# Kernel tuning notes

Measured on AMD Instinct MI355X. Metric: run time of the kernel, lower is better.

The kernel has to match this reference:

```python
import jax, jax.numpy as jnp
import numpy as np

N_NODES = 100000

def gcn_conv(x, edge_index, W, b, n_nodes):
    # GCNConv: out = D^{-1/2} (A + I) D^{-1/2} X W + b  (self-loops added)
    src, dst = edge_index[0], edge_index[1]
    loops = jnp.arange(n_nodes, dtype=edge_index.dtype)
    src = jnp.concatenate([src, loops])
    dst = jnp.concatenate([dst, loops])
    deg = jax.ops.segment_sum(jnp.ones_like(dst, dtype=x.dtype), dst, num_segments=n_nodes)
    dinv = jnp.where(deg > 0, jax.lax.rsqrt(deg), 0.0)
    norm = dinv[src] * dinv[dst]  # [E+N]
    h = x @ W  # transform first (small d), then gather/scatter
    msgs = h[src] * norm[:, None]
    out = jax.ops.segment_sum(msgs, dst, num_segments=n_nodes)
    return out + b


def setup_inputs() -> dict:
    key = jax.random.key(0)
    k1, k2, k3, k4, k5, k6 = jax.random.split(key, 6)
    x = jax.random.normal(k1, (N_NODES, 3), dtype=jnp.float32)
    edge_index = jax.random.randint(k2, (2, 2400000), 0, N_NODES, dtype=jnp.int64)
    # Glorot-style init for GCNConv linear weights; zero bias matches PyG default
    W1 = jax.random.normal(k3, (3, 16), dtype=jnp.float32) * (1.0 / np.sqrt(3))
    b1 = jnp.zeros((16,), dtype=jnp.float32)
    W2 = jax.random.normal(k4, (16, 32), dtype=jnp.float32) * (1.0 / np.sqrt(16))
    b2 = jnp.zeros((32,), dtype=jnp.float32)
    return {"x": x, "edge_index": edge_index, "W1": W1, "b1": b1, "W2": W2, "b2": b2}


def reference(x, edge_index, W1, b1, W2, b2):
    n = x.shape[0]
    h = gcn_conv(x, edge_index, W1, b1, n)
    h = jax.nn.relu(h)
    h = gcn_conv(h, edge_index, W2, b2, n)
    # batch is all zeros in the original forward -> single-graph mean pool
    return jnp.mean(h, axis=0, keepdims=True)  # [1, 32]
```

## Files before the change

### kernel.cpp

```cpp
#include <hip/hip_runtime.h>

typedef unsigned int uint;
typedef unsigned long long ull;


#define MAXB  256
#define CAP   16384u
#define BINB  512
#define CHUNK 4096
#define SPL   8
#define PADN  131072
#define AFS   2048.0f
#define AFB   16384
#define AFM   0x1FFFFFu

__device__ __forceinline__ uint slice_lo(uint c, uint s) {
    return (s == 0u) ? 0u : ((c * s / SPL) & ~7u);
}
__device__ __forceinline__ uint slice_hi(uint c, uint s) {
    return (s == SPL - 1u) ? c : ((c * (s + 1u) / SPL) & ~7u);
}

__global__ void __launch_bounds__(BINB)
bin_kernel(const int* __restrict__ key, const int* __restrict__ other,
           uint* __restrict__ cursor, uint* __restrict__ buf, int E) {
    __shared__ uint cnt[MAXB], scanb[MAXB], baseb[MAXB];
    __shared__ uint stage[CHUNK];
    const int tid = threadIdx.x;
    const int e0 = blockIdx.x * CHUNK;
    const int nE = min(CHUNK, E - e0);
    const int my0 = tid * 8;
    const int myc = max(0, min(8, nE - my0));
    if (tid < MAXB) cnt[tid] = 0u;

    uint k8[8], o8[8], r8[8];
    if (myc == 8) {
        int4 ka = ((const int4*)(key + e0))[tid * 2];
        int4 kb = ((const int4*)(key + e0))[tid * 2 + 1];
        int4 oa = ((const int4*)(other + e0))[tid * 2];
        int4 ob = ((const int4*)(other + e0))[tid * 2 + 1];
        k8[0] = ka.x; k8[1] = ka.y; k8[2] = ka.z; k8[3] = ka.w;
        k8[4] = kb.x; k8[5] = kb.y; k8[6] = kb.z; k8[7] = kb.w;
        o8[0] = oa.x; o8[1] = oa.y; o8[2] = oa.z; o8[3] = oa.w;
        o8[4] = ob.x; o8[5] = ob.y; o8[6] = ob.z; o8[7] = ob.w;
    } else {
        for (int r = 0; r < myc; ++r) {
            k8[r] = (uint)key[e0 + my0 + r];
            o8[r] = (uint)other[e0 + my0 + r];
        }
    }
    __syncthreads();
    for (int r = 0; r < myc; ++r) r8[r] = atomicAdd(&cnt[k8[r] >> 9], 1u);
    __syncthreads();
    if (tid < MAXB) scanb[tid] = cnt[tid];
    __syncthreads();
    for (int d = 1; d < MAXB; d <<= 1) {
        uint t = (tid < MAXB && tid >= d) ? scanb[tid - d] : 0u;
        __syncthreads();
        if (tid < MAXB) scanb[tid] += t;
        __syncthreads();
    }
    if (tid < MAXB) baseb[tid] = (uint)tid * CAP + (cnt[tid] ? atomicAdd(&cursor[tid * 16], cnt[tid]) : 0u);
    __syncthreads();
    for (int r = 0; r < myc; ++r) {
        uint b = k8[r] >> 9;
        stage[(scanb[b] - cnt[b]) + r8[r]] = ((k8[r] & 511u) << 17) | o8[r];
    }
    __syncthreads();
    const int wave = tid >> 6, lane = tid & 63;
    for (int b = wave; b < MAXB; b += BINB / 64) {
        uint s0 = scanb[b] - cnt[b], c = cnt[b], gb = baseb[b];
        uint lim = (uint)(b + 1) * CAP;
        for (uint i = lane; i < c; i += 64u) {
            uint gp = gb + i;
            if (gp < lim) buf[gp] = stage[s0 + i];
        }
    }
}

__global__ void __launch_bounds__(256)
deg_kernel(const uint* __restrict__ buf, const uint* __restrict__ curD,
           uint* __restrict__ degg, int n) {
    __shared__ uint dg[512];
    const int tid = threadIdx.x;
    const int b = blockIdx.x >> 3;
    const uint s = blockIdx.x & 7;
    const uint base = (uint)b * CAP;
    const uint c = min(curD[b * 16], CAP);
    const uint lo = slice_lo(c, s), hi = slice_hi(c, s);
    dg[tid] = 0u; dg[tid + 256] = 0u;
    __syncthreads();
    for (uint i0 = lo + (uint)tid * 8u; i0 < hi; i0 += 2048u) {
        uint cnt8 = min(8u, hi - i0);
        uint en[8];
        if (cnt8 == 8u) {
            uint4 a = ((const uint4*)(buf + base + i0))[0];
            uint4 bb = ((const uint4*)(buf + base + i0))[1];
            en[0] = a.x; en[1] = a.y; en[2] = a.z; en[3] = a.w;
            en[4] = bb.x; en[5] = bb.y; en[6] = bb.z; en[7] = bb.w;
        } else {
            for (uint r = 0; r < cnt8; ++r) en[r] = buf[base + i0 + r];
        }
        for (uint r = 0; r < cnt8; ++r) atomicAdd(&dg[en[r] >> 17], 1u);
    }
    __syncthreads();
    for (int t = tid; t < 512; t += 256) {
        int node = (b << 9) + t;
        if (node < n && dg[t]) atomicAdd(&degg[node], dg[t]);
    }
}

__global__ void node1_kernel(const float* __restrict__ x, const uint* __restrict__ degg,
                             float* __restrict__ dinv, float4* __restrict__ xd4, int n) {
    int i = blockIdx.x * blockDim.x + threadIdx.x;
    if (i >= n) return;
    float di = rsqrtf((float)(degg[i] + 1u));
    dinv[i] = di;
    xd4[i] = make_float4(x[3 * i] * di, x[3 * i + 1] * di, x[3 * i + 2] * di, di);
}

__global__ void __launch_bounds__(256)
agg_kernel(const uint* __restrict__ buf, const uint* __restrict__ curD,
           const float4* __restrict__ xd4, ull* __restrict__ accp, int n) {
    __shared__ ull acc[512];
    const int tid = threadIdx.x;
    const int b = blockIdx.x >> 3;
    const uint s = blockIdx.x & 7;
    const uint base = (uint)b * CAP;
    const uint c = min(curD[b * 16], CAP);
    const uint lo = slice_lo(c, s), hi = slice_hi(c, s);
    acc[tid] = 0ull; acc[tid + 256] = 0ull;
    __syncthreads();
    for (uint i0 = lo + (uint)tid * 8u; i0 < hi + 8u * 2048u; i0 += 2048u) {
        if (i0 >= hi) continue;
        uint cnt8 = min(8u, hi - i0);
        uint en[8];
        if (cnt8 == 8u) {
            uint4 a = ((const uint4*)(buf + base + i0))[0];
            uint4 bb = ((const uint4*)(buf + base + i0))[1];
            en[0] = a.x; en[1] = a.y; en[2] = a.z; en[3] = a.w;
            en[4] = bb.x; en[5] = bb.y; en[6] = bb.z; en[7] = bb.w;
        } else {
            for (uint r = 0; r < cnt8; ++r) en[r] = buf[base + i0 + r];
            for (uint r = cnt8; r < 8u; ++r) en[r] = en[0];
        }
        float4 gv[8];
#pragma unroll
        for (int r = 0; r < 8; ++r) gv[r] = xd4[en[r] & 0x1FFFFu];
#pragma unroll
        for (uint r = 0; r < 8u; ++r) {
            if (r < cnt8) {
                uint dl = en[r] >> 17;
                ull f0 = (ull)(uint)((int)rintf(gv[r].x * AFS) + AFB);
                ull f1 = (ull)(uint)((int)rintf(gv[r].y * AFS) + AFB);
                ull f2 = (ull)(uint)((int)rintf(gv[r].z * AFS) + AFB);
                atomicAdd(&acc[dl], f0 | (f1 << 21) | (f2 << 42));
            }
        }
    }
    __syncthreads();
    for (int t = tid; t < 512; t += 256) {
        ull v = acc[t];
        int node = (b << 9) + t;
        if (v && node < n) atomicAdd(&accp[node], v);
    }
}

__global__ void __launch_bounds__(256)
q_kernel(const ull* __restrict__ accp, const uint* __restrict__ degg,
         const float4* __restrict__ xd4, const float* __restrict__ W1,
         const float* __restrict__ b1, uint4* __restrict__ qb,
         float* __restrict__ T, int n) {
    __shared__ float tacc[16];
    const int tid = threadIdx.x;
    if (tid < 16) tacc[tid] = 0.0f;
    __syncthreads();
    int i = blockIdx.x * blockDim.x + tid;
    float sq[16];
    if (i < n) {
        float4 sv = xd4[i];
        float di = sv.w;
        ull v = accp[i];
        int ub = (int)(degg[i] * (uint)AFB);
        const float isc = 1.0f / AFS;
        float a = (float)((int)(uint)(v & AFM) - ub) * isc + sv.x;
        float b = (float)((int)(uint)((v >> 21) & AFM) - ub) * isc + sv.y;
        float c = (float)((int)(uint)((v >> 42) & AFM) - ub) * isc + sv.z;
        float q[16];
#pragma unroll
        for (int k = 0; k < 16; ++k) {
            float h = di * (a * W1[k] + b * W1[16 + k] + c * W1[32 + k]) + b1[k];
            h = fmaxf(h, 0.0f);
            q[k] = di * h;
            sq[k] = di * q[k];
        }
        uint pk[8];
#pragma unroll
        for (int k = 0; k < 8; ++k) {
            uint l = __float_as_uint(q[2 * k]);
            l = (l + 0x7FFFu + ((l >> 16) & 1u)) >> 16;
            uint h2 = __float_as_uint(q[2 * k + 1]);
            h2 = ((h2 + 0x7FFFu + ((h2 >> 16) & 1u)) & 0xFFFF0000u);
            pk[k] = l | h2;
        }
        qb[2 * (size_t)i]     = make_uint4(pk[0], pk[1], pk[2], pk[3]);
        qb[2 * (size_t)i + 1] = make_uint4(pk[4], pk[5], pk[6], pk[7]);
    } else {
#pragma unroll
        for (int k = 0; k < 16; ++k) sq[k] = 0.0f;
    }
#pragma unroll
    for (int k = 0; k < 16; ++k) {
        float v = sq[k];
        for (int off = 32; off > 0; off >>= 1) v += __shfl_down(v, off, 64);
        if ((tid & 63) == 0) atomicAdd(&tacc[k], v);
    }
    __syncthreads();
    if (tid < 16) atomicAdd(&T[tid], tacc[tid]);
}

__global__ void __launch_bounds__(256)
T_kernel(const uint* __restrict__ buf, const uint* __restrict__ curD,
         const float* __restrict__ dinv, const uint4* __restrict__ qb,
         float* __restrict__ T, int n) {
    __shared__ float dt[512];
    __shared__ float tacc[16];
    const int tid = threadIdx.x;
    const int b = blockIdx.x >> 3;
    const uint s = blockIdx.x & 7;
    const uint base = (uint)b * CAP;
    const uint c = min(curD[b * 16], CAP);
    const uint lo = slice_lo(c, s), hi = slice_hi(c, s);
    for (int t = tid; t < 512; t += 256) {
        int node = (b << 9) + t;
        dt[t] = (node < n) ? dinv[node] : 0.0f;
    }
    if (tid < 16) tacc[tid] = 0.0f;
    __syncthreads();
    float rac[16];
#pragma unroll
    for (int k = 0; k < 16; ++k) rac[k] = 0.0f;
    for (uint i0 = lo + (uint)tid * 8u; i0 < hi + 8u * 2048u; i0 += 2048u) {
        if (i0 >= hi) continue;
        uint cnt8 = min(8u, hi - i0);
        uint en[8];
        if (cnt8 == 8u) {
            uint4 a = ((const uint4*)(buf + base + i0))[0];
            uint4 bb = ((const uint4*)(buf + base + i0))[1];
            en[0] = a.x; en[1] = a.y; en[2] = a.z; en[3] = a.w;
            en[4] = bb.x; en[5] = bb.y; en[6] = bb.z; en[7] = bb.w;
        } else {
            for (uint r = 0; r < cnt8; ++r) en[r] = buf[base + i0 + r];
            for (uint r = cnt8; r < 8u; ++r) en[r] = en[0];
        }
        uint4 qa[8], qc[8];
#pragma unroll
        for (int r = 0; r < 8; ++r) {
            uint sv = en[r] & 0x1FFFFu;
            qa[r] = qb[2 * (size_t)sv];
            qc[r] = qb[2 * (size_t)sv + 1];
        }
#pragma unroll
        for (uint r = 0; r < 8u; ++r) {
            if (r < cnt8) {
                float di = dt[en[r] >> 17];
                uint w[8] = {qa[r].x, qa[r].y, qa[r].z, qa[r].w,
                             qc[r].x, qc[r].y, qc[r].z, qc[r].w};
#pragma unroll
                for (int k = 0; k < 8; ++k) {
                    rac[2 * k]     += di * __uint_as_float(w[k] << 16);
                    rac[2 * k + 1] += di * __uint_as_float(w[k] & 0xFFFF0000u);
                }
            }
        }
    }
#pragma unroll
    for (int k = 0; k < 16; ++k) {
        float v = rac[k];
        for (int off = 32; off > 0; off >>= 1) v += __shfl_down(v, off, 64);
        if ((tid & 63) == 0) atomicAdd(&tacc[k], v);
    }
    __syncthreads();
    if (tid < 16) atomicAdd(&T[tid], tacc[tid]);
}

__global__ void out_kernel(const float* __restrict__ T, const float* __restrict__ W2,
                           const float* __restrict__ b2, float* __restrict__ out, float invN) {
    int j = threadIdx.x;
    float s = 0.0f;
#pragma unroll
    for (int k = 0; k < 16; ++k) s += T[k] * W2[k * 32 + j];
    out[j] = b2[j] + invN * s;
}

extern "C" void kernel_launch(void* const* d_in, const int* in_sizes, int n_in,
                              void* d_out, int out_size, void* d_ws, size_t ws_size,
                              hipStream_t stream) {
    const float* x   = (const float*)d_in[0];
    const int*   ei  = (const int*)d_in[1];
    const float* W1  = (const float*)d_in[2];
    const float* b1  = (const float*)d_in[3];
    const float* W2  = (const float*)d_in[4];
    const float* b2  = (const float*)d_in[5];
    float* out = (float*)d_out;

    const int n = in_sizes[0] / 3;
    const int E = in_sizes[1] / 2;
    const int* src = ei;
    const int* dst = ei + E;

    char* p = (char*)d_ws;
    float* T    = (float*)p;    p += 64;
    uint*  curD = (uint*)p;     p += MAXB * 16 * 4;
    uint*  degg = (uint*)p;     p += (size_t)n * 4;
    ull*   accp = (ull*)p;      p += (size_t)n * 8;
    size_t zbytes = (size_t)(p - (char*)d_ws);
    uint*   bufD  = (uint*)p;   p += (size_t)MAXB * CAP * 4;
    float*  dinv  = (float*)p;  p += (size_t)n * 4;
    p = (char*)(((size_t)p + 31) & ~(size_t)31);
    float4* xd4   = (float4*)p; p += (size_t)PADN * 16;
    uint4*  qb    = (uint4*)p;  p += (size_t)PADN * 32;

    const int nb = (n + 511) >> 9;

    hipMemsetAsync(d_ws, 0, zbytes, stream);
    bin_kernel<<<(E + CHUNK - 1) / CHUNK, BINB, 0, stream>>>(dst, src, curD, bufD, E);
    deg_kernel<<<nb * SPL, 256, 0, stream>>>(bufD, curD, degg, n);
    node1_kernel<<<(n + 255) / 256, 256, 0, stream>>>(x, degg, dinv, xd4, n);
    agg_kernel<<<nb * SPL, 256, 0, stream>>>(bufD, curD, xd4, accp, n);
    q_kernel<<<(n + 255) / 256, 256, 0, stream>>>(accp, degg, xd4, W1, b1, qb, T, n);
    T_kernel<<<nb * SPL, 256, 0, stream>>>(bufD, curD, dinv, qb, T, n);
    out_kernel<<<1, 32, 0, stream>>>(T, W2, b2, out, 1.0f / (float)n);
}
```

Measured before the change: 166.7 us.

## Fuse degree with node prep and aggregation with layer-1 transform via whole-bin blocks

```diff
diff --git a/kernel.cpp b/kernel.cpp
--- a/kernel.cpp
+++ b/kernel.cpp
@@ -9,10 +9,10 @@
 #define BINB  512
 #define CHUNK 4096
 #define SPL   8
-#define PADN  131072
 #define AFS   2048.0f
 #define AFB   16384
 #define AFM   0x1FFFFFu
+#define PADN  131072
 
 __device__ __forceinline__ uint slice_lo(uint c, uint s) {
     return (s == 0u) ? 0u : ((c * s / SPL) & ~7u);
@@ -78,20 +78,19 @@
     }
 }
 
-__global__ void __launch_bounds__(256)
-deg_kernel(const uint* __restrict__ buf, const uint* __restrict__ curD,
-           uint* __restrict__ degg, int n) {
+__global__ void __launch_bounds__(1024)
+degnode_kernel(const uint* __restrict__ buf, const uint* __restrict__ curD,
+               const float* __restrict__ x, uint* __restrict__ degg,
+               float* __restrict__ dinv, float4* __restrict__ xd4, int n) {
     __shared__ uint dg[512];
     const int tid = threadIdx.x;
-    const int b = blockIdx.x >> 3;
-    const uint s = blockIdx.x & 7;
+    const int b = blockIdx.x;
     const uint base = (uint)b * CAP;
     const uint c = min(curD[b * 16], CAP);
-    const uint lo = slice_lo(c, s), hi = slice_hi(c, s);
-    dg[tid] = 0u; dg[tid + 256] = 0u;
-    __syncthreads();
-    for (uint i0 = lo + (uint)tid * 8u; i0 < hi; i0 += 2048u) {
-        uint cnt8 = min(8u, hi - i0);
+    if (tid < 512) dg[tid] = 0u;
+    __syncthreads();
+    for (uint i0 = (uint)tid * 8u; i0 < c; i0 += 8192u) {
+        uint cnt8 = min(8u, c - i0);
         uint en[8];
         if (cnt8 == 8u) {
             uint4 a = ((const uint4*)(buf + base + i0))[0];
@@ -104,36 +103,35 @@
         for (uint r = 0; r < cnt8; ++r) atomicAdd(&dg[en[r] >> 17], 1u);
     }
     __syncthreads();
-    for (int t = tid; t < 512; t += 256) {
-        int node = (b << 9) + t;
-        if (node < n && dg[t]) atomicAdd(&degg[node], dg[t]);
-    }
-}
-
-__global__ void node1_kernel(const float* __restrict__ x, const uint* __restrict__ degg,
-                             float* __restrict__ dinv, float4* __restrict__ xd4, int n) {
-    int i = blockIdx.x * blockDim.x + threadIdx.x;
-    if (i >= n) return;
-    float di = rsqrtf((float)(degg[i] + 1u));
-    dinv[i] = di;
-    xd4[i] = make_float4(x[3 * i] * di, x[3 * i + 1] * di, x[3 * i + 2] * di, di);
-}
-
-__global__ void __launch_bounds__(256)
-agg_kernel(const uint* __restrict__ buf, const uint* __restrict__ curD,
-           const float4* __restrict__ xd4, ull* __restrict__ accp, int n) {
+    if (tid < 512) {
+        int node = (b << 9) + tid;
+        if (node < n) {
+            uint d = dg[tid];
+            degg[node] = d;
+            float di = rsqrtf((float)(d + 1u));
+            dinv[node] = di;
+            xd4[node] = make_float4(x[3 * node] * di, x[3 * node + 1] * di,
+                                    x[3 * node + 2] * di, di);
+        }
+    }
+}
+
+__global__ void __launch_bounds__(1024)
+aggq_kernel(const uint* __restrict__ buf, const uint* __restrict__ curD,
+            const uint* __restrict__ degg, const float4* __restrict__ xd4,
+            const float* __restrict__ W1, const float* __restrict__ b1,
+            uint4* __restrict__ qb, float* __restrict__ T, int n) {
     __shared__ ull acc[512];
+    __shared__ float taccs[16];
     const int tid = threadIdx.x;
-    const int b = blockIdx.x >> 3;
-    const uint s = blockIdx.x & 7;
+    const int b = blockIdx.x;
     const uint base = (uint)b * CAP;
     const uint c = min(curD[b * 16], CAP);
-    const uint lo = slice_lo(c, s), hi = slice_hi(c, s);
-    acc[tid] = 0ull; acc[tid + 256] = 0ull;
-    __syncthreads();
-    for (uint i0 = lo + (uint)tid * 8u; i0 < hi + 8u * 2048u; i0 += 2048u) {
-        if (i0 >= hi) continue;
-        uint cnt8 = min(8u, hi - i0);
+    if (tid < 512) acc[tid] = 0ull;
+    if (tid < 16) taccs[tid] = 0.0f;
+    __syncthreads();
+    for (uint i0 = (uint)tid * 8u; i0 < c; i0 += 8192u) {
+        uint cnt8 = min(8u, c - i0);
         uint en[8];
         if (cnt8 == 8u) {
             uint4 a = ((const uint4*)(buf + base + i0))[0];
@@ -159,64 +157,51 @@
         }
     }
     __syncthreads();
-    for (int t = tid; t < 512; t += 256) {
-        ull v = acc[t];
-        int node = (b << 9) + t;
-        if (v && node < n) atomicAdd(&accp[node], v);
-    }
-}
-
-__global__ void __launch_bounds__(256)
-q_kernel(const ull* __restrict__ accp, const uint* __restrict__ degg,
-         const float4* __restrict__ xd4, const float* __restrict__ W1,
-         const float* __restrict__ b1, uint4* __restrict__ qb,
-         float* __restrict__ T, int n) {
-    __shared__ float tacc[16];
-    const int tid = threadIdx.x;
-    if (tid < 16) tacc[tid] = 0.0f;
-    __syncthreads();
-    int i = blockIdx.x * blockDim.x + tid;
     float sq[16];
-    if (i < n) {
-        float4 sv = xd4[i];
-        float di = sv.w;
-        ull v = accp[i];
-        int ub = (int)(degg[i] * (uint)AFB);
-        const float isc = 1.0f / AFS;
-        float a = (float)((int)(uint)(v & AFM) - ub) * isc + sv.x;
-        float b = (float)((int)(uint)((v >> 21) & AFM) - ub) * isc + sv.y;
-        float c = (float)((int)(uint)((v >> 42) & AFM) - ub) * isc + sv.z;
-        float q[16];
+#pragma unroll
+    for (int k = 0; k < 16; ++k) sq[k] = 0.0f;
+    if (tid < 512) {
+        int node = (b << 9) + tid;
+        if (node < n) {
+            ull v = acc[tid];
+            int ub = (int)(degg[node] * (uint)AFB);
+            float4 sv = xd4[node];
+            float di = sv.w;
+            const float isc = 1.0f / AFS;
+            float av = (float)((int)(uint)(v & AFM) - ub) * isc + sv.x;
+            float bv = (float)((int)(uint)((v >> 21) & AFM) - ub) * isc + sv.y;
+            float cv = (float)((int)(uint)((v >> 42) & AFM) - ub) * isc + sv.z;
+            float q[16];
+#pragma unroll
+            for (int k = 0; k < 16; ++k) {
+                float h = di * (av * W1[k] + bv * W1[16 + k] + cv * W1[32 + k]) + b1[k];
+                h = fmaxf(h, 0.0f);
+                q[k] = di * h;
+                sq[k] = di * q[k];
+            }
+            uint pk[8];
+#pragma unroll
+            for (int k = 0; k < 8; ++k) {
+                uint l = __float_as_uint(q[2 * k]);
+                l = (l + 0x7FFFu + ((l >> 16) & 1u)) >> 16;
+                uint h2 = __float_as_uint(q[2 * k + 1]);
+                h2 = ((h2 + 0x7FFFu + ((h2 >> 16) & 1u)) & 0xFFFF0000u);
+                pk[k] = l | h2;
+            }
+            qb[2 * (size_t)node]     = make_uint4(pk[0], pk[1], pk[2], pk[3]);
+            qb[2 * (size_t)node + 1] = make_uint4(pk[4], pk[5], pk[6], pk[7]);
+        }
+    }
+    if (tid < 512) {
 #pragma unroll
         for (int k = 0; k < 16; ++k) {
-            float h = di * (a * W1[k] + b * W1[16 + k] + c * W1[32 + k]) + b1[k];
-            h = fmaxf(h, 0.0f);
-            q[k] = di * h;
-            sq[k] = di * q[k];
-        }
-        uint pk[8];
-#pragma unroll
-        for (int k = 0; k < 8; ++k) {
-            uint l = __float_as_uint(q[2 * k]);
-            l = (l + 0x7FFFu + ((l >> 16) & 1u)) >> 16;
-            uint h2 = __float_as_uint(q[2 * k + 1]);
-            h2 = ((h2 + 0x7FFFu + ((h2 >> 16) & 1u)) & 0xFFFF0000u);
-            pk[k] = l | h2;
-        }
-        qb[2 * (size_t)i]     = make_uint4(pk[0], pk[1], pk[2], pk[3]);
-        qb[2 * (size_t)i + 1] = make_uint4(pk[4], pk[5], pk[6], pk[7]);
-    } else {
-#pragma unroll
-        for (int k = 0; k < 16; ++k) sq[k] = 0.0f;
-    }
-#pragma unroll
-    for (int k = 0; k < 16; ++k) {
-        float v = sq[k];
-        for (int off = 32; off > 0; off >>= 1) v += __shfl_down(v, off, 64);
-        if ((tid & 63) == 0) atomicAdd(&tacc[k], v);
-    }
-    __syncthreads();
-    if (tid < 16) atomicAdd(&T[tid], tacc[tid]);
+            float v = sq[k];
+            for (int off = 32; off > 0; off >>= 1) v += __shfl_down(v, off, 64);
+            if ((tid & 63) == 0) atomicAdd(&taccs[k], v);
+        }
+    }
+    __syncthreads();
+    if (tid < 16) atomicAdd(&T[tid], taccs[tid]);
 }
 
 __global__ void __launch_bounds__(256)
@@ -312,23 +297,20 @@
     char* p = (char*)d_ws;
     float* T    = (float*)p;    p += 64;
     uint*  curD = (uint*)p;     p += MAXB * 16 * 4;
-    uint*  degg = (uint*)p;     p += (size_t)n * 4;
-    ull*   accp = (ull*)p;      p += (size_t)n * 8;
     size_t zbytes = (size_t)(p - (char*)d_ws);
-    uint*   bufD  = (uint*)p;   p += (size_t)MAXB * CAP * 4;
-    float*  dinv  = (float*)p;  p += (size_t)n * 4;
+    uint*  degg  = (uint*)p;    p += (size_t)n * 4;
+    uint*  bufD  = (uint*)p;    p += (size_t)MAXB * CAP * 4;
+    float* dinv  = (float*)p;   p += (size_t)n * 4;
     p = (char*)(((size_t)p + 31) & ~(size_t)31);
-    float4* xd4   = (float4*)p; p += (size_t)PADN * 16;
-    uint4*  qb    = (uint4*)p;  p += (size_t)PADN * 32;
+    float4* xd4  = (float4*)p;  p += (size_t)PADN * 16;
+    uint4*  qb   = (uint4*)p;   p += (size_t)PADN * 32;
 
     const int nb = (n + 511) >> 9;
 
     hipMemsetAsync(d_ws, 0, zbytes, stream);
     bin_kernel<<<(E + CHUNK - 1) / CHUNK, BINB, 0, stream>>>(dst, src, curD, bufD, E);
-    deg_kernel<<<nb * SPL, 256, 0, stream>>>(bufD, curD, degg, n);
-    node1_kernel<<<(n + 255) / 256, 256, 0, stream>>>(x, degg, dinv, xd4, n);
-    agg_kernel<<<nb * SPL, 256, 0, stream>>>(bufD, curD, xd4, accp, n);
-    q_kernel<<<(n + 255) / 256, 256, 0, stream>>>(accp, degg, xd4, W1, b1, qb, T, n);
+    degnode_kernel<<<nb, 1024, 0, stream>>>(bufD, curD, x, degg, dinv, xd4, n);
+    aggq_kernel<<<nb, 1024, 0, stream>>>(bufD, curD, degg, xd4, W1, b1, qb, T, n);
     T_kernel<<<nb * SPL, 256, 0, stream>>>(bufD, curD, dinv, qb, T, n);
     out_kernel<<<1, 32, 0, stream>>>(T, W2, b2, out, 1.0f / (float)n);
 }
```

New measurement: 158.7 us. 1.05x faster.
